# Optimization experiments

Measured on AMD Instinct MI355X. Metric: run time of the kernel, lower is better.

Reference implementation:

```python
import jax, jax.numpy as jnp
import numpy as np

N_NODES = 10000
N_EDGES = 80000
N_GRAPHS = 64
H, D = 4, 512          # num_heads, out_feats
EMB = 768
HFEAT = 512
NCLS = 2
SLOPE = 0.2            # DGL GATConv default negative_slope
BN_EPS = 1e-5


def setup_inputs() -> dict:
    key = jax.random.key(0)
    ks = jax.random.split(key, 24)
    f32 = jnp.float32
    rn = lambda k, s, sc=0.02: jax.random.normal(k, s, dtype=f32) * sc
    inp = {
        "node_feat": jax.random.normal(ks[0], (N_NODES, EMB), dtype=f32),
        "func_feat": jax.random.normal(ks[1], (N_NODES, EMB), dtype=f32),
        "W1": rn(ks[2], (EMB, H * D)),
        "al1": rn(ks[3], (H, D), 0.1),
        "ar1": rn(ks[4], (H, D), 0.1),
        "b1": jnp.zeros((H * D,), f32),
        "W2": rn(ks[5], (H * D, H * D)),
        "al2": rn(ks[6], (H, D), 0.1),
        "ar2": rn(ks[7], (H, D), 0.1),
        "b2": jnp.zeros((H * D,), f32),
        "Wfc": rn(ks[8], (H * D, HFEAT)),
        "bfc": jnp.zeros((HFEAT,), f32),
        "Wfco": rn(ks[9], (EMB, HFEAT)),
        "bfco": jnp.zeros((HFEAT,), f32),
        "Wh": rn(ks[10], (8, HFEAT, HFEAT)),
        "bh": jnp.zeros((8, HFEAT), f32),
        "gamma": jnp.ones((HFEAT,), f32),
        "beta": jnp.zeros((HFEAT,), f32),
        "Whfc": rn(ks[11], (HFEAT, HFEAT)),
        "bhfc": jnp.zeros((HFEAT,), f32),
        "Wf": rn(ks[12], (HFEAT, NCLS)),
        "bf": jnp.zeros((NCLS,), f32),
        "src": jax.random.randint(ks[13], (N_EDGES,), 0, N_NODES),
        "dst": jax.random.randint(ks[14], (N_EDGES,), 0, N_NODES),
        "graph_id": jnp.sort(jax.random.randint(ks[15], (N_NODES,), 0, N_GRAPHS)),
    }
    return inp


def gat_conv(h, W, al, ar, b, src, dst):
    """DGL GATConv (eval mode): fc -> per-head attention logits -> edge
    softmax over incoming edges -> scatter-sum -> +bias. Returns (N, H*D)."""
    feat = (h @ W).reshape(-1, H, D)                      # (N,H,D)
    el = jnp.einsum('nhd,hd->nh', feat, al)               # (N,H)
    er = jnp.einsum('nhd,hd->nh', feat, ar)
    e = jax.nn.leaky_relu(el[src] + er[dst], SLOPE)       # (E,H)
    emax = jax.ops.segment_max(e, dst, num_segments=N_NODES)
    ex = jnp.exp(e - emax[dst])
    den = jax.ops.segment_sum(ex, dst, num_segments=N_NODES)
    a = ex / den[dst]                                     # edge softmax (E,H)
    msg = feat[src] * a[:, :, None]                       # (E,H,D) gather+weight
    out = jax.ops.segment_sum(msg, dst, num_segments=N_NODES)
    return (out + b.reshape(1, H, D)).reshape(-1, H * D)


def reference(node_feat, func_feat, W1, al1, ar1, b1, W2, al2, ar2, b2,
              Wfc, bfc, Wfco, bfco, Wh, bh, gamma, beta, Whfc, bhfc,
              Wf, bf, src, dst, graph_id):
    h = gat_conv(node_feat, W1, al1, ar1, b1, src, dst)   # (N, 2048)
    h = gat_conv(h, W2, al2, ar2, b2, src, dst)           # (N, 2048)
    h = jax.nn.elu(h @ Wfc + bfc)                         # (N, 512)
    h_func = jax.nn.elu(func_feat @ Wfco + bfco)          # (N, 512)
    for i in range(8):
        h = jax.nn.elu(h @ Wh[i] + bh[i])
        h_func = jax.nn.elu(h_func @ Wh[i] + bh[i])       # dead for output (as in torch)
    counts = jax.ops.segment_sum(jnp.ones((N_NODES,), h.dtype), graph_id,
                                 num_segments=N_GRAPHS)
    hg = jax.ops.segment_sum(h, graph_id, num_segments=N_GRAPHS)
    hg = hg / jnp.maximum(counts, 1.0)[:, None]           # dgl.mean_nodes (G, 512)
    # BatchNorm1d eval with running_mean=0, running_var=1
    hg = hg / jnp.sqrt(1.0 + BN_EPS) * gamma + beta
    hg = jax.nn.elu(hg @ Whfc + bhfc)
    return hg @ Wf + bf                                   # (G, NCLS)
```

## Files before the change

kernel.cpp:

```cpp
#include <hip/hip_runtime.h>
#include <hip/hip_bf16.h>
#include <math.h>

#define N_NODES 10000
#define N_EDGES 80000
#define N_GRAPHS 64
#define NH 4
#define HD 512
#define HDTOT 2048
#define EMB 768
#define HFEAT 512
#define MAXDEG 512

typedef _Float16 half8 __attribute__((ext_vector_type(8)));
typedef _Float16 half4 __attribute__((ext_vector_type(4)));
typedef float f32x4 __attribute__((ext_vector_type(4)));

__device__ __forceinline__ void gload_lds16(const void* g, void* l) {
  __builtin_amdgcn_global_load_lds(
      (const __attribute__((address_space(1))) unsigned int*)g,
      (__attribute__((address_space(3))) unsigned int*)l, 16, 0, 0);
}

__device__ __forceinline__ void wgbar() {
  asm volatile("" ::: "memory");
  __builtin_amdgcn_s_barrier();
  asm volatile("" ::: "memory");
}

template <int N>
__device__ __forceinline__ void vmwait() {
  asm volatile("s_waitcnt vmcnt(%0)" ::"n"(N) : "memory");
}

template <int BM>
__global__ __launch_bounds__(256) void gemm_f16_kernel(
    const _Float16* __restrict__ A, const _Float16* __restrict__ BT,
    const float* __restrict__ bias, _Float16* __restrict__ C,
    int M, int N, int K, int act) {
  constexpr int WR = (BM == 128) ? 2 : 1;
  constexpr int WC = 4 / WR;
  constexpr int MI = (BM / WR) / 16;
  constexpr int NI = (128 / WC) / 16;
  constexpr int NW = NI * 16;
  constexpr int CS = NW + 4;
  constexpr int GPR = NW / 8;

  __shared__ _Float16 smem[(BM + 128) * 64];
  _Float16* As = smem;
  _Float16* Bs = smem + BM * 64;

  const int bn = blockIdx.x * 128, bm = blockIdx.y * BM;
  const int t = threadIdx.x;
  const int lane = t & 63, wave = t >> 6;
  const int wr = wave / WC, wc = wave % WC;
  const int m0 = wr * (BM / WR), n0 = wc * NW;
  const int fr = lane & 15, fq = lane >> 4;

  f32x4 acc[MI][NI];
#pragma unroll
  for (int i = 0; i < MI; ++i)
#pragma unroll
    for (int j = 0; j < NI; ++j) acc[i][j] = (f32x4){0.f, 0.f, 0.f, 0.f};

  for (int k0 = 0; k0 < K; k0 += 64) {
    __syncthreads();
#pragma unroll
    for (int it = 0; it < BM / 32; ++it) {
      int gid = it * 256 + t;
      int r = gid >> 3;
      int q = (gid & 7) ^ (r & 7);
      int grow = bm + r;
      if (grow >= M) grow = M - 1;
      gload_lds16(A + (size_t)grow * K + k0 + q * 8,
                  &As[(it * 256 + wave * 64) * 8]);
    }
#pragma unroll
    for (int it = 0; it < 4; ++it) {
      int gid = it * 256 + t;
      int r = gid >> 3;
      int q = (gid & 7) ^ (r & 7);
      gload_lds16(BT + (size_t)(bn + r) * K + k0 + q * 8,
                  &Bs[(it * 256 + wave * 64) * 8]);
    }
    __syncthreads();

#pragma unroll
    for (int kk = 0; kk < 2; ++kk) {
      half8 af[MI], bf[NI];
#pragma unroll
      for (int mi = 0; mi < MI; ++mi) {
        int m = m0 + mi * 16 + fr;
        af[mi] = *(const half8*)&As[m * 64 + (((kk * 4 + fq) ^ (m & 7))) * 8];
      }
#pragma unroll
      for (int ni = 0; ni < NI; ++ni) {
        int n = n0 + ni * 16 + fr;
        bf[ni] = *(const half8*)&Bs[n * 64 + (((kk * 4 + fq) ^ (n & 7))) * 8];
      }
#pragma unroll
      for (int mi = 0; mi < MI; ++mi)
#pragma unroll
        for (int ni = 0; ni < NI; ++ni)
          acc[mi][ni] = __builtin_amdgcn_mfma_f32_16x16x32_f16(
              af[mi], bf[ni], acc[mi][ni], 0, 0, 0);
    }
  }
  __syncthreads();
  _Float16* cs = smem + wave * 16 * CS;
#pragma unroll
  for (int mi = 0; mi < MI; ++mi) {
#pragma unroll
    for (int ni = 0; ni < NI; ++ni) {
      float bb = bias ? bias[bn + n0 + ni * 16 + fr] : 0.f;
#pragma unroll
      for (int j = 0; j < 4; ++j) {
        float v = acc[mi][ni][j] + bb;
        if (act == 1) v = v > 0.f ? v : expm1f(v);
        cs[(fq * 4 + j) * CS + ni * 16 + fr] = (_Float16)v;
      }
    }
#pragma unroll
    for (int i = 0; i < NW / 32; ++i) {
      int piece = i * 64 + lane;
      int r = piece / GPR, g = piece % GPR;
      int grow = bm + m0 + mi * 16 + r;
      if (grow < M) {
        half8 v = *(const half8*)&cs[r * CS + g * 8];
        *(half8*)&C[(size_t)grow * N + bn + n0 + g * 8] = v;
      }
    }
  }
}

#define G256_SLOT 16384

__global__ __launch_bounds__(512, 2) void gemm256_f16_kernel(
    const _Float16* __restrict__ A, const _Float16* __restrict__ BT,
    const float* __restrict__ bias, _Float16* __restrict__ C,
    int M, int N, int K, int act, int nbx) {
  __shared__ _Float16 smem[4 * G256_SLOT];

  int flat = blockIdx.x;
  int nwg = gridDim.x;
  if ((nwg & 7) == 0) flat = (flat & 7) * (nwg >> 3) + (flat >> 3);
  const int bn = (flat % nbx) * 256;
  const int bm = (flat / nbx) * 256;

  const int t = threadIdx.x;
  const int lane = t & 63, wave = t >> 6;
  const int wr = wave >> 2, wc = wave & 3;
  const int m0 = wr * 128, n0 = wc * 64;
  const int fr = lane & 15, fq = lane >> 4;

  const _Float16* srcA[2];
  const _Float16* srcB[2];
#pragma unroll
  for (int it = 0; it < 2; ++it) {
    int gi = it * 512 + t;
    int r = gi >> 2;
    int g = (gi & 3) ^ ((r >> 1) & 3);
    int ra = bm + r;
    if (ra >= M) ra = M - 1;
    srcA[it] = A + (size_t)ra * K + g * 8;
    srcB[it] = BT + (size_t)(bn + r) * K + g * 8;
  }

  int offA[8], offB[4];
#pragma unroll
  for (int mi = 0; mi < 8; ++mi) {
    int m = m0 + mi * 16 + fr;
    offA[mi] = m * 32 + ((fq ^ ((m >> 1) & 3)) << 3);
  }
#pragma unroll
  for (int ni = 0; ni < 4; ++ni) {
    int n = n0 + ni * 16 + fr;
    offB[ni] = 8192 + n * 32 + ((fq ^ ((n >> 1) & 3)) << 3);
  }

  f32x4 acc[8][4];
#pragma unroll
  for (int i = 0; i < 8; ++i)
#pragma unroll
    for (int j = 0; j < 4; ++j) acc[i][j] = (f32x4){0.f, 0.f, 0.f, 0.f};

  const int ldsbase = (wave * 64) * 8;

#define G256_STAGE(kt, slot)                                               \
  do {                                                                     \
    _Float16* sA_ = smem + (slot)*G256_SLOT;                               \
    _Float16* sB_ = sA_ + 8192;                                            \
    gload_lds16(srcA[0] + (size_t)(kt)*32, &sA_[ldsbase]);                 \
    gload_lds16(srcA[1] + (size_t)(kt)*32, &sA_[4096 + ldsbase]);          \
    gload_lds16(srcB[0] + (size_t)(kt)*32, &sB_[ldsbase]);                 \
    gload_lds16(srcB[1] + (size_t)(kt)*32, &sB_[4096 + ldsbase]);          \
  } while (0)

  const int NT = K >> 5;

  G256_STAGE(0, 0);
  G256_STAGE(1, 1);
  G256_STAGE(2, 2);
  vmwait<8>();
  wgbar();

  for (int tt = 0; tt < NT; ++tt) {
    if (tt + 3 < NT) G256_STAGE(tt + 3, (tt + 3) & 3);

    const _Float16* sl = smem + (tt & 3) * G256_SLOT;
    half8 af[8], bf[4];
#pragma unroll
    for (int mi = 0; mi < 8; ++mi) af[mi] = *(const half8*)&sl[offA[mi]];
#pragma unroll
    for (int ni = 0; ni < 4; ++ni) bf[ni] = *(const half8*)&sl[offB[ni]];

    __builtin_amdgcn_s_setprio(1);
#pragma unroll
    for (int mi = 0; mi < 8; ++mi)
#pragma unroll
      for (int ni = 0; ni < 4; ++ni)
        acc[mi][ni] = __builtin_amdgcn_mfma_f32_16x16x32_f16(
            af[mi], bf[ni], acc[mi][ni], 0, 0, 0);
    __builtin_amdgcn_s_setprio(0);

    if (tt + 3 < NT)
      vmwait<8>();
    else if (tt + 2 < NT)
      vmwait<4>();
    else if (tt + 1 < NT)
      vmwait<0>();
    wgbar();
  }
#undef G256_STAGE

  constexpr int CS = 68;
  _Float16* cs = smem + wave * 16 * CS;
#pragma unroll
  for (int mi = 0; mi < 8; ++mi) {
#pragma unroll
    for (int ni = 0; ni < 4; ++ni) {
      float bb = bias ? bias[bn + n0 + ni * 16 + fr] : 0.f;
#pragma unroll
      for (int j = 0; j < 4; ++j) {
        float v = acc[mi][ni][j] + bb;
        if (act == 1) v = v > 0.f ? v : expm1f(v);
        cs[(fq * 4 + j) * CS + ni * 16 + fr] = (_Float16)v;
      }
    }
#pragma unroll
    for (int i = 0; i < 2; ++i) {
      int piece = i * 64 + lane;
      int r = piece >> 3, g = piece & 7;
      int grow = bm + m0 + mi * 16 + r;
      if (grow < M) {
        half8 v = *(const half8*)&cs[r * CS + g * 8];
        *(half8*)&C[(size_t)grow * N + bn + n0 + g * 8] = v;
      }
    }
  }
}

__global__ __launch_bounds__(256) void convert_wt_kernel(
    const float* __restrict__ W, _Float16* __restrict__ WT, int K, int N) {
  __shared__ float tile[32][33];
  W += (size_t)blockIdx.z * K * N;
  WT += (size_t)blockIdx.z * K * N;
  int k0 = blockIdx.x * 32, n0 = blockIdx.y * 32;
  int t = threadIdx.x;
  int r = t >> 3, c4 = (t & 7) * 4;
  float4 v = *(const float4*)(W + (size_t)(k0 + r) * N + n0 + c4);
  tile[r][c4 + 0] = v.x;
  tile[r][c4 + 1] = v.y;
  tile[r][c4 + 2] = v.z;
  tile[r][c4 + 3] = v.w;
  __syncthreads();
  float x0 = tile[c4 + 0][r], x1 = tile[c4 + 1][r];
  float x2 = tile[c4 + 2][r], x3 = tile[c4 + 3][r];
  size_t o = (size_t)(n0 + r) * K + k0 + c4;
  *(half4*)&WT[o] = (half4){(_Float16)x0, (_Float16)x1, (_Float16)x2, (_Float16)x3};
}

__global__ void convert_f32_f16_kernel(const float* __restrict__ x,
                                       _Float16* __restrict__ y, int n4) {
  int gid = blockIdx.x * blockDim.x + threadIdx.x;
  if (gid >= n4) return;
  float4 v = *(const float4*)(x + gid * 4);
  *(half4*)(y + gid * 4) =
      (half4){(_Float16)v.x, (_Float16)v.y, (_Float16)v.z, (_Float16)v.w};
}

__global__ void hist_kernel(const int* __restrict__ dst, int* __restrict__ cnt, int E) {
  int gid = blockIdx.x * blockDim.x + threadIdx.x;
  if (gid < E) atomicAdd(&cnt[dst[gid]], 1);
}

__global__ void scan_kernel(const int* __restrict__ cnt, int* __restrict__ row_ptr,
                            int* __restrict__ cursor, int n) {
  __shared__ int part[256];
  int t = threadIdx.x;
  int chunk = (n + 255) / 256;
  int s0 = t * chunk;
  int s1 = min(s0 + chunk, n);
  int sum = 0;
  for (int i = s0; i < s1; ++i) sum += cnt[i];
  part[t] = sum;
  __syncthreads();
  if (t == 0) {
    int acc = 0;
    for (int i = 0; i < 256; ++i) { int v = part[i]; part[i] = acc; acc += v; }
    row_ptr[n] = acc;
  }
  __syncthreads();
  int run = part[t];
  for (int i = s0; i < s1; ++i) {
    row_ptr[i] = run;
    cursor[i] = run;
    run += cnt[i];
  }
}

__global__ void scatter_kernel(const int* __restrict__ src, const int* __restrict__ dst,
                               int* __restrict__ cursor, int* __restrict__ csr_src,
                               int E) {
  int gid = blockIdx.x * blockDim.x + threadIdx.x;
  if (gid < E) {
    int d = dst[gid];
    int pos = atomicAdd(&cursor[d], 1);
    csr_src[pos] = src[gid];
  }
}

__global__ __launch_bounds__(256) void el_er_kernel(
    const _Float16* __restrict__ feat, const float* __restrict__ al,
    const float* __restrict__ ar, float* __restrict__ el, float* __restrict__ er) {
  int n = blockIdx.x;
  int t = threadIdx.x;
  int h = t >> 6, lane = t & 63;
  half8 f = *(const half8*)(feat + (size_t)n * HDTOT + h * HD + lane * 8);
  const float* ap = al + h * HD + lane * 8;
  const float* rp = ar + h * HD + lane * 8;
  float4 a0 = *(const float4*)ap, a1 = *(const float4*)(ap + 4);
  float4 r0 = *(const float4*)rp, r1 = *(const float4*)(rp + 4);
  float f0 = (float)f[0], f1 = (float)f[1], f2 = (float)f[2], f3 = (float)f[3];
  float f4 = (float)f[4], f5 = (float)f[5], f6 = (float)f[6], f7 = (float)f[7];
  float sl = f0 * a0.x + f1 * a0.y + f2 * a0.z + f3 * a0.w +
             f4 * a1.x + f5 * a1.y + f6 * a1.z + f7 * a1.w;
  float sr = f0 * r0.x + f1 * r0.y + f2 * r0.z + f3 * r0.w +
             f4 * r1.x + f5 * r1.y + f6 * r1.z + f7 * r1.w;
  for (int off = 32; off; off >>= 1) {
    sl += __shfl_down(sl, off);
    sr += __shfl_down(sr, off);
  }
  if (lane == 0) {
    el[n * NH + h] = sl;
    er[n * NH + h] = sr;
  }
}

__global__ __launch_bounds__(256) void softmax_aggregate_kernel(
    const _Float16* __restrict__ feat, const float* __restrict__ el,
    const float* __restrict__ er, const int* __restrict__ row_ptr,
    const int* __restrict__ csr_src, float* __restrict__ e_buf,
    const float* __restrict__ bias, _Float16* __restrict__ out) {
  __shared__ float wl[NH][MAXDEG];
  int n = blockIdx.x;
  int t = threadIdx.x;
  int h = t >> 6, lane = t & 63;
  int s = row_ptr[n], epos = row_ptr[n + 1];
  int deg = epos - s;
  bool lds_w = (deg <= MAXDEG);

  if (deg > 0) {
    float ern = er[n * NH + h];
    if (deg <= 64) {
      int p = s + lane;
      bool on = lane < deg;
      float logit = 0.f;
      float m = -INFINITY;
      if (on) {
        float v = el[csr_src[p] * NH + h] + ern;
        logit = v >= 0.f ? v : 0.2f * v;
        m = logit;
      }
#pragma unroll
      for (int off = 32; off; off >>= 1) m = fmaxf(m, __shfl_xor(m, off));
      float ex = on ? expf(logit - m) : 0.f;
      float sum = ex;
#pragma unroll
      for (int off = 32; off; off >>= 1) sum += __shfl_xor(sum, off);
      float inv = 1.f / sum;
      if (on) wl[h][lane] = ex * inv;
    } else if (lds_w) {
      float m = -INFINITY;
      for (int p = s + lane; p < epos; p += 64) {
        float v = el[csr_src[p] * NH + h] + ern;
        v = v >= 0.f ? v : 0.2f * v;
        wl[h][p - s] = v;
        m = fmaxf(m, v);
      }
      for (int off = 32; off; off >>= 1) m = fmaxf(m, __shfl_xor(m, off));
      float sum = 0.f;
      for (int p = s + lane; p < epos; p += 64) {
        float ex = expf(wl[h][p - s] - m);
        wl[h][p - s] = ex;
        sum += ex;
      }
      for (int off = 32; off; off >>= 1) sum += __shfl_xor(sum, off);
      float inv = 1.f / sum;
      for (int p = s + lane; p < epos; p += 64) wl[h][p - s] *= inv;
    } else {
      float m = -INFINITY;
      for (int p = s + lane; p < epos; p += 64) {
        float v = el[csr_src[p] * NH + h] + ern;
        v = v >= 0.f ? v : 0.2f * v;
        e_buf[p * NH + h] = v;
        m = fmaxf(m, v);
      }
      for (int off = 32; off; off >>= 1) m = fmaxf(m, __shfl_xor(m, off));
      float sum = 0.f;
      for (int p = s + lane; p < epos; p += 64) {
        float ex = expf(e_buf[p * NH + h] - m);
        e_buf[p * NH + h] = ex;
        sum += ex;
      }
      for (int off = 32; off; off >>= 1) sum += __shfl_xor(sum, off);
      float inv = 1.f / sum;
      for (int p = s + lane; p < epos; p += 64) e_buf[p * NH + h] *= inv;
    }
  }
  __syncthreads();

  int base = t * 8;
  float acc[8] = {0.f, 0.f, 0.f, 0.f, 0.f, 0.f, 0.f, 0.f};
  int p = s;
  for (; p + 4 <= epos; p += 4) {
    int q = p - s;
    int sn0 = csr_src[p + 0], sn1 = csr_src[p + 1];
    int sn2 = csr_src[p + 2], sn3 = csr_src[p + 3];
    float a0 = lds_w ? wl[h][q + 0] : e_buf[(p + 0) * NH + h];
    float a1 = lds_w ? wl[h][q + 1] : e_buf[(p + 1) * NH + h];
    float a2 = lds_w ? wl[h][q + 2] : e_buf[(p + 2) * NH + h];
    float a3 = lds_w ? wl[h][q + 3] : e_buf[(p + 3) * NH + h];
    half8 f0 = *(const half8*)(feat + (size_t)sn0 * HDTOT + base);
    half8 f1 = *(const half8*)(feat + (size_t)sn1 * HDTOT + base);
    half8 f2 = *(const half8*)(feat + (size_t)sn2 * HDTOT + base);
    half8 f3 = *(const half8*)(feat + (size_t)sn3 * HDTOT + base);
#pragma unroll
    for (int i = 0; i < 8; ++i)
      acc[i] += a0 * (float)f0[i] + a1 * (float)f1[i] +
                a2 * (float)f2[i] + a3 * (float)f3[i];
  }
  for (; p < epos; ++p) {
    int sn = csr_src[p];
    float a = lds_w ? wl[h][p - s] : e_buf[p * NH + h];
    half8 f = *(const half8*)(feat + (size_t)sn * HDTOT + base);
#pragma unroll
    for (int i = 0; i < 8; ++i) acc[i] += a * (float)f[i];
  }
  float4 b0 = *(const float4*)(bias + base);
  float4 b1 = *(const float4*)(bias + base + 4);
  half8 o;
  o[0] = (_Float16)(acc[0] + b0.x); o[1] = (_Float16)(acc[1] + b0.y);
  o[2] = (_Float16)(acc[2] + b0.z); o[3] = (_Float16)(acc[3] + b0.w);
  o[4] = (_Float16)(acc[4] + b1.x); o[5] = (_Float16)(acc[5] + b1.y);
  o[6] = (_Float16)(acc[6] + b1.z); o[7] = (_Float16)(acc[7] + b1.w);
  *(half8*)(out + (size_t)n * HDTOT + base) = o;
}

__global__ __launch_bounds__(512) void pool_final_kernel(
    const _Float16* __restrict__ hfeat, const int* __restrict__ graph_id,
    const float* __restrict__ gamma, const float* __restrict__ beta,
    const float* __restrict__ Whfc, const float* __restrict__ bhfc,
    const float* __restrict__ Wf, const float* __restrict__ bf,
    float* __restrict__ out) {
  __shared__ float sh[HFEAT];
  __shared__ float st[HFEAT];
  __shared__ float r0[8], r1[8];
  __shared__ int s_lo, s_hi;
  int g = blockIdx.x, t = threadIdx.x;
  if (t == 0) {
    int lo = 0, hi = N_NODES;
    while (lo < hi) { int m = (lo + hi) >> 1; if (graph_id[m] < g) lo = m + 1; else hi = m; }
    s_lo = lo;
    int lo2 = lo, hi2 = N_NODES;
    while (lo2 < hi2) { int m = (lo2 + hi2) >> 1; if (graph_id[m] < g + 1) lo2 = m + 1; else hi2 = m; }
    s_hi = lo2;
  }
  __syncthreads();
  int lo = s_lo, hi = s_hi;
  int col = t;
  float acc = 0.f;
  for (int n = lo; n < hi; ++n) acc += (float)hfeat[(size_t)n * HFEAT + col];
  float invc = 1.f / fmaxf((float)(hi - lo), 1.f);
  float bnscale = rsqrtf(1.f + 1e-5f);
  sh[col] = acc * invc * bnscale * gamma[col] + beta[col];
  __syncthreads();
  float a2 = bhfc[col];
  for (int k = 0; k < HFEAT; ++k) a2 += sh[k] * Whfc[k * HFEAT + col];
  st[col] = a2 > 0.f ? a2 : expm1f(a2);
  __syncthreads();
  float p0 = st[col] * Wf[col * 2 + 0];
  float p1 = st[col] * Wf[col * 2 + 1];
  for (int off = 32; off; off >>= 1) {
    p0 += __shfl_down(p0, off);
    p1 += __shfl_down(p1, off);
  }
  int w = t >> 6;
  if ((t & 63) == 0) { r0[w] = p0; r1[w] = p1; }
  __syncthreads();
  if (t == 0) {
    float q0 = bf[0], q1 = bf[1];
#pragma unroll
    for (int i = 0; i < 8; ++i) { q0 += r0[i]; q1 += r1[i]; }
    out[g * 2 + 0] = q0;
    out[g * 2 + 1] = q1;
  }
}

static void gemm_raw(const _Float16* A, const _Float16* wt, const float* bias,
                     _Float16* C, int M, int N, int K, int act,
                     bool small_m_tile, hipStream_t stream) {
  if (small_m_tile) {
    dim3 grid(N / 128, (M + 63) / 64);
    hipLaunchKernelGGL(gemm_f16_kernel<64>, grid, dim3(256), 0, stream,
                       A, wt, bias, C, M, N, K, act);
  } else {
    dim3 grid(N / 128, (M + 127) / 128);
    hipLaunchKernelGGL(gemm_f16_kernel<128>, grid, dim3(256), 0, stream,
                       A, wt, bias, C, M, N, K, act);
  }
}

static void gemm(const _Float16* A, const float* W, _Float16* wt,
                 const float* bias, _Float16* C, int M, int N, int K, int act,
                 bool small_m_tile, hipStream_t stream) {
  hipLaunchKernelGGL(convert_wt_kernel, dim3(K / 32, N / 32, 1), dim3(256),
                     0, stream, W, wt, K, N);
  gemm_raw(A, wt, bias, C, M, N, K, act, small_m_tile, stream);
}

static void gemm_big(const _Float16* A, const float* W, _Float16* wt,
                     const float* bias, _Float16* C, int M, int N, int K,
                     int act, hipStream_t stream) {
  hipLaunchKernelGGL(convert_wt_kernel, dim3(K / 32, N / 32, 1), dim3(256),
                     0, stream, W, wt, K, N);
  int nbx = N / 256, nby = (M + 255) / 256;
  hipLaunchKernelGGL(gemm256_f16_kernel, dim3(nbx * nby), dim3(512), 0, stream,
                     A, wt, bias, C, M, N, K, act, nbx);
}

static void gat_layer(const _Float16* h_in, int K_in, const float* W, _Float16* wt,
                      const float* al, const float* ar, const float* b,
                      const int* row_ptr, const int* csr_src,
                      _Float16* featbuf, float* el, float* er,
                      float* e_buf, _Float16* out, hipStream_t stream) {
  gemm_big(h_in, W, wt, nullptr, featbuf, N_NODES, HDTOT, K_in, 0, stream);
  hipLaunchKernelGGL(el_er_kernel, dim3(N_NODES), dim3(256), 0, stream, featbuf, al, ar, el, er);
  hipLaunchKernelGGL(softmax_aggregate_kernel, dim3(N_NODES), dim3(256), 0, stream,
                     featbuf, el, er, row_ptr, csr_src, e_buf, b, out);
}

extern "C" void kernel_launch(void* const* d_in, const int* in_sizes, int n_in,
                              void* d_out, int out_size, void* d_ws, size_t ws_size,
                              hipStream_t stream) {
  const float* node_feat = (const float*)d_in[0];
  const float* W1 = (const float*)d_in[2];
  const float* al1 = (const float*)d_in[3];
  const float* ar1 = (const float*)d_in[4];
  const float* b1 = (const float*)d_in[5];
  const float* W2 = (const float*)d_in[6];
  const float* al2 = (const float*)d_in[7];
  const float* ar2 = (const float*)d_in[8];
  const float* b2 = (const float*)d_in[9];
  const float* Wfc = (const float*)d_in[10];
  const float* bfc = (const float*)d_in[11];
  const float* Wh = (const float*)d_in[14];
  const float* bh = (const float*)d_in[15];
  const float* gamma = (const float*)d_in[16];
  const float* beta = (const float*)d_in[17];
  const float* Whfc = (const float*)d_in[18];
  const float* bhfc = (const float*)d_in[19];
  const float* Wf = (const float*)d_in[20];
  const float* bf = (const float*)d_in[21];
  const int* src = (const int*)d_in[22];
  const int* dst = (const int*)d_in[23];
  const int* graph_id = (const int*)d_in[24];
  float* out = (float*)d_out;

  _Float16* P0 = (_Float16*)d_ws;
  _Float16* P1 = P0 + (size_t)N_NODES * HDTOT;
  _Float16* Pin = P1 + (size_t)N_NODES * HDTOT;
  _Float16* wt = Pin + (size_t)N_NODES * EMB;
  _Float16* whh = wt + (size_t)2048 * 2048;
  float* el = (float*)(whh + (size_t)8 * HFEAT * HFEAT);
  float* er = el + N_NODES * NH;
  float* e_buf = er + N_NODES * NH;
  int* cnt = (int*)(e_buf + (size_t)N_EDGES * NH);
  int* row_ptr = cnt + N_NODES;
  int* cursor = row_ptr + N_NODES + 1;
  int* csr_src = cursor + N_NODES;

  hipMemsetAsync(cnt, 0, N_NODES * sizeof(int), stream);
  hipLaunchKernelGGL(hist_kernel, dim3((N_EDGES + 255) / 256), dim3(256), 0, stream,
                     dst, cnt, N_EDGES);
  hipLaunchKernelGGL(scan_kernel, dim3(1), dim3(256), 0, stream, cnt, row_ptr, cursor, N_NODES);
  hipLaunchKernelGGL(scatter_kernel, dim3((N_EDGES + 255) / 256), dim3(256), 0, stream,
                     src, dst, cursor, csr_src, N_EDGES);

  int n4 = N_NODES * EMB / 4;
  hipLaunchKernelGGL(convert_f32_f16_kernel, dim3((n4 + 255) / 256), dim3(256), 0, stream,
                     node_feat, Pin, n4);
  hipLaunchKernelGGL(convert_wt_kernel, dim3(HFEAT / 32, HFEAT / 32, 8),
                     dim3(256), 0, stream, Wh, whh, HFEAT, HFEAT);

  gat_layer(Pin, EMB, W1, wt, al1, ar1, b1, row_ptr, csr_src,
            P0, el, er, e_buf, P1, stream);
  gat_layer(P1, HDTOT, W2, wt, al2, ar2, b2, row_ptr, csr_src,
            P0, el, er, e_buf, P1, stream);

  gemm(P1, Wfc, wt, bfc, P0, N_NODES, HFEAT, HDTOT, 1, true, stream);

  _Float16* cur = P0;
  _Float16* nxt = P1;
  for (int i = 0; i < 8; ++i) {
    gemm_raw(cur, whh + (size_t)i * HFEAT * HFEAT, bh + (size_t)i * HFEAT, nxt,
             N_NODES, HFEAT, HFEAT, 1, true, stream);
    _Float16* tmp = cur; cur = nxt; nxt = tmp;
  }

  hipLaunchKernelGGL(pool_final_kernel, dim3(N_GRAPHS), dim3(512), 0, stream,
                     cur, graph_id, gamma, beta, Whfc, bhfc, Wf, bf, out);
}
```

Before: 729.4 us.

## Restructure 256x256 GEMM into ping-pong half-stage pipeline and split M into exact tiles

Replaces the 4-slot, K=32 pipelined 256x256 GEMM with a two-buffer K=64 scheme that issues loads in quarter-stages interleaved with four MFMA phases per iteration. Occupancy drops to one workgroup per CU. The launcher runs this kernel on exactly 256 tiles covering the first 8192 rows, which matches the 256 CUs, and sends the remaining rows to the 128-tile GEMM kernel. The aim is better load/MFMA overlap and no partial wave of tiles, at the cost of an extra launch and more barriers per iteration.

```diff
diff --git a/kernel.cpp b/kernel.cpp
--- a/kernel.cpp
+++ b/kernel.cpp
@@ -133,13 +133,13 @@
   }
 }
 
-#define G256_SLOT 16384
-
-__global__ __launch_bounds__(512, 2) void gemm256_f16_kernel(
+#define GP_SLOT 8192
+
+__global__ __launch_bounds__(512, 1) void gemm256p_f16_kernel(
     const _Float16* __restrict__ A, const _Float16* __restrict__ BT,
     const float* __restrict__ bias, _Float16* __restrict__ C,
     int M, int N, int K, int act, int nbx) {
-  __shared__ _Float16 smem[4 * G256_SLOT];
+  __shared__ _Float16 smem[8 * GP_SLOT];
 
   int flat = blockIdx.x;
   int nwg = gridDim.x;
@@ -153,8 +153,8 @@
   const int m0 = wr * 128, n0 = wc * 64;
   const int fr = lane & 15, fq = lane >> 4;
 
-  const _Float16* srcA[2];
-  const _Float16* srcB[2];
+  const _Float16* sA[2];
+  const _Float16* sB[2];
 #pragma unroll
   for (int it = 0; it < 2; ++it) {
     int gi = it * 512 + t;
@@ -162,9 +162,10 @@
     int g = (gi & 3) ^ ((r >> 1) & 3);
     int ra = bm + r;
     if (ra >= M) ra = M - 1;
-    srcA[it] = A + (size_t)ra * K + g * 8;
-    srcB[it] = BT + (size_t)(bn + r) * K + g * 8;
-  }
+    sA[it] = A + (size_t)ra * K + g * 8;
+    sB[it] = BT + (size_t)(bn + r) * K + g * 8;
+  }
+  const int ldsbase = (wave * 64) * 8;
 
   int offA[8], offB[4];
 #pragma unroll
@@ -175,7 +176,7 @@
 #pragma unroll
   for (int ni = 0; ni < 4; ++ni) {
     int n = n0 + ni * 16 + fr;
-    offB[ni] = 8192 + n * 32 + ((fq ^ ((n >> 1) & 3)) << 3);
+    offB[ni] = n * 32 + ((fq ^ ((n >> 1) & 3)) << 3);
   }
 
   f32x4 acc[8][4];
@@ -184,54 +185,66 @@
 #pragma unroll
     for (int j = 0; j < 4; ++j) acc[i][j] = (f32x4){0.f, 0.f, 0.f, 0.f};
 
-  const int ldsbase = (wave * 64) * 8;
-
-#define G256_STAGE(kt, slot)                                               \
-  do {                                                                     \
-    _Float16* sA_ = smem + (slot)*G256_SLOT;                               \
-    _Float16* sB_ = sA_ + 8192;                                            \
-    gload_lds16(srcA[0] + (size_t)(kt)*32, &sA_[ldsbase]);                 \
-    gload_lds16(srcA[1] + (size_t)(kt)*32, &sA_[4096 + ldsbase]);          \
-    gload_lds16(srcB[0] + (size_t)(kt)*32, &sB_[ldsbase]);                 \
-    gload_lds16(srcB[1] + (size_t)(kt)*32, &sB_[4096 + ldsbase]);          \
+#define STAGE_HALF(kt, wh)                                                  \
+  do {                                                                      \
+    _Float16* dst_ = smem + ((((kt)&1) * 4 + (wh)) * GP_SLOT);              \
+    const _Float16* s0_ = ((wh)&1) ? sB[0] : sA[0];                         \
+    const _Float16* s1_ = ((wh)&1) ? sB[1] : sA[1];                         \
+    size_t ko_ = (size_t)(kt)*64 + (((wh) >> 1) * 32);                      \
+    gload_lds16(s0_ + ko_, &dst_[ldsbase]);                                 \
+    gload_lds16(s1_ + ko_, &dst_[4096 + ldsbase]);                          \
   } while (0)
 
-  const int NT = K >> 5;
-
-  G256_STAGE(0, 0);
-  G256_STAGE(1, 1);
-  G256_STAGE(2, 2);
-  vmwait<8>();
+#define PHASE_MFMA(Ah, Bh, MB)                                              \
+  do {                                                                      \
+    half8 af_[4], bf_[4];                                                   \
+    _Pragma("unroll") for (int i_ = 0; i_ < 4; ++i_)                        \
+        af_[i_] = *(const half8*)&(Ah)[offA[(MB) + i_]];                    \
+    _Pragma("unroll") for (int n_ = 0; n_ < 4; ++n_)                        \
+        bf_[n_] = *(const half8*)&(Bh)[offB[n_]];                           \
+    __builtin_amdgcn_s_setprio(1);                                          \
+    _Pragma("unroll") for (int i_ = 0; i_ < 4; ++i_)                        \
+        _Pragma("unroll") for (int n_ = 0; n_ < 4; ++n_)                    \
+            acc[(MB) + i_][n_] = __builtin_amdgcn_mfma_f32_16x16x32_f16(    \
+                af_[i_], bf_[n_], acc[(MB) + i_][n_], 0, 0, 0);             \
+    __builtin_amdgcn_s_setprio(0);                                          \
+  } while (0)
+
+  const int NT = K >> 6;
+
+  STAGE_HALF(0, 0);
+  STAGE_HALF(0, 1);
+  STAGE_HALF(0, 2);
+  STAGE_HALF(0, 3);
+  vmwait<4>();
   wgbar();
 
   for (int tt = 0; tt < NT; ++tt) {
-    if (tt + 3 < NT) G256_STAGE(tt + 3, (tt + 3) & 3);
-
-    const _Float16* sl = smem + (tt & 3) * G256_SLOT;
-    half8 af[8], bf[4];
-#pragma unroll
-    for (int mi = 0; mi < 8; ++mi) af[mi] = *(const half8*)&sl[offA[mi]];
-#pragma unroll
-    for (int ni = 0; ni < 4; ++ni) bf[ni] = *(const half8*)&sl[offB[ni]];
-
-    __builtin_amdgcn_s_setprio(1);
-#pragma unroll
-    for (int mi = 0; mi < 8; ++mi)
-#pragma unroll
-      for (int ni = 0; ni < 4; ++ni)
-        acc[mi][ni] = __builtin_amdgcn_mfma_f32_16x16x32_f16(
-            af[mi], bf[ni], acc[mi][ni], 0, 0, 0);
-    __builtin_amdgcn_s_setprio(0);
-
-    if (tt + 3 < NT)
-      vmwait<8>();
-    else if (tt + 2 < NT)
-      vmwait<4>();
-    else if (tt + 1 < NT)
-      vmwait<0>();
+    const bool more = (tt + 1 < NT);
+    const _Float16* base = smem + (tt & 1) * 4 * GP_SLOT;
+    const _Float16* A0 = base;
+    const _Float16* B0 = base + GP_SLOT;
+    const _Float16* A1 = base + 2 * GP_SLOT;
+    const _Float16* B1 = base + 3 * GP_SLOT;
+
+    if (more) STAGE_HALF(tt + 1, 0);
+    PHASE_MFMA(A0, B0, 0);
     wgbar();
-  }
-#undef G256_STAGE
+    if (more) STAGE_HALF(tt + 1, 1);
+    PHASE_MFMA(A0, B0, 4);
+    if (more) vmwait<4>();
+    else vmwait<0>();
+    wgbar();
+    if (more) STAGE_HALF(tt + 1, 2);
+    PHASE_MFMA(A1, B1, 0);
+    wgbar();
+    if (more) STAGE_HALF(tt + 1, 3);
+    PHASE_MFMA(A1, B1, 4);
+    if (more) vmwait<4>();
+    wgbar();
+  }
+#undef STAGE_HALF
+#undef PHASE_MFMA
 
   constexpr int CS = 68;
   _Float16* cs = smem + wave * 16 * CS;
@@ -544,9 +557,18 @@
                      int act, hipStream_t stream) {
   hipLaunchKernelGGL(convert_wt_kernel, dim3(K / 32, N / 32, 1), dim3(256),
                      0, stream, W, wt, K, N);
-  int nbx = N / 256, nby = (M + 255) / 256;
-  hipLaunchKernelGGL(gemm256_f16_kernel, dim3(nbx * nby), dim3(512), 0, stream,
-                     A, wt, bias, C, M, N, K, act, nbx);
+  if (N == 2048 && M > 8192 && (K & 63) == 0) {
+    int nbx = N / 256;
+    hipLaunchKernelGGL(gemm256p_f16_kernel, dim3(256), dim3(512), 0, stream,
+                       A, wt, bias, C, 8192, N, K, act, nbx);
+    int rem = M - 8192;
+    dim3 grid(N / 128, (rem + 127) / 128);
+    hipLaunchKernelGGL(gemm_f16_kernel<128>, grid, dim3(256), 0, stream,
+                       A + (size_t)8192 * K, wt, bias,
+                       C + (size_t)8192 * N, rem, N, K, act);
+  } else {
+    gemm_raw(A, wt, bias, C, M, N, K, act, false, stream);
+  }
 }
 
 static void gat_layer(const _Float16* h_in, int K_in, const float* W, _Float16* wt,
```

Result: no change. 738.0 us (+1.2%).
